# Optimization experiments

Hardware: AMD Instinct MI355X
Metric: run time of the kernel (lower is better)

Reference implementation:

```python
import jax, jax.numpy as jnp
import numpy as np

B, S, D = 4, 2048, 1024
H, ADIM = 16, 64
HID = H * ADIM  # 1024


def setup_inputs() -> dict:
    key = jax.random.key(0)
    k1, k2, k3, k4 = jax.random.split(key, 4)
    iQ = jax.random.normal(k1, (B, S, D), dtype=jnp.float32)
    mask = jax.random.randint(k2, (B, S, S), 0, 2).astype(bool)
    Wa = jax.random.normal(k3, (3 * HID, D), dtype=jnp.float32) * (1.0 / np.sqrt(D))
    Wo = jax.random.normal(k4, (HID, HID), dtype=jnp.float32) * (1.0 / np.sqrt(HID))
    return {"iQ": iQ, "mask": mask, "Wa": Wa, "Wo": Wo}


def reference(iQ, mask, Wa, Wo):
    b, s, _ = iQ.shape
    # fused QKV projection: [B,S,3*HID]
    qkv = jnp.einsum("bsd,ed->bse", iQ, Wa)
    q, k, v = jnp.split(qkv, 3, axis=-1)
    # [B,S,HID] -> [B,H,S,ADIM]
    to_heads = lambda t: t.reshape(b, s, H, ADIM).transpose(0, 2, 1, 3)
    q, k, v = to_heads(q), to_heads(k), to_heads(v)
    scores = jnp.einsum("bhqd,bhkd->bhqk", q, k) / np.sqrt(ADIM).astype(np.float32)
    scores = jnp.where(mask[:, None, :, :], jnp.float32(-1e32), scores)
    attn = jax.nn.softmax(scores, axis=-1)
    o = jnp.einsum("bhqk,bhkd->bhqd", attn, v)
    o = o.transpose(0, 2, 1, 3).reshape(b, s, HID)
    return jnp.einsum("bse,oe->bso", o, Wo)
```

## Files before the change

kernel.cpp:

```cpp
#include <hip/hip_runtime.h>
#include <hip/hip_bf16.h>

typedef __bf16 bf16;
typedef __bf16 bfrag __attribute__((ext_vector_type(8)));
typedef __bf16 bf16x2 __attribute__((ext_vector_type(2)));
typedef float f32x4 __attribute__((ext_vector_type(4)));
typedef float f32x16 __attribute__((ext_vector_type(16)));
typedef unsigned u32x2 __attribute__((ext_vector_type(2)));

constexpr int Bc = 4, Sc = 2048, Hc = 16, ADc = 64, HIDc = 1024;
constexpr size_t QKV_ELEMS = (size_t)Bc * Hc * Sc * ADc;

__device__ __forceinline__ void gload_lds16(const void* g, void* lds) {
  __builtin_amdgcn_global_load_lds(
      (const __attribute__((address_space(1))) unsigned int*)g,
      (__attribute__((address_space(3))) unsigned int*)lds, 16, 0, 0);
}

__device__ __forceinline__ bfrag ldb(const bf16* p) {
  return *(const bfrag*)p;
}

__device__ __forceinline__ unsigned pack2(float lo, float hi) {
  union { bf16x2 h; unsigned u; } c;
  c.h = bf16x2{(bf16)lo, (bf16)hi};
  return c.u;
}

__device__ __forceinline__ void plswap(unsigned& a, unsigned& b) {
  u32x2 r = __builtin_amdgcn_permlane32_swap(a, b, false, false);
  a = r.x;
  b = r.y;
}

__device__ __forceinline__ f32x16 zero16() {
  f32x16 z;
#pragma unroll
  for (int i = 0; i < 16; ++i) z[i] = 0.f;
  return z;
}

__global__ __launch_bounds__(256) void prep(const float* __restrict__ s0,
                                            const float* __restrict__ s1,
                                            const float* __restrict__ s2,
                                            bf16* __restrict__ d0,
                                            bf16* __restrict__ d1,
                                            bf16* __restrict__ d2,
                                            const int* __restrict__ mask,
                                            unsigned* __restrict__ bits) {
  const int blk = blockIdx.x;
  if (blk < 6144) {
    const float* s;
    bf16* d;
    size_t base;
    if (blk < 4096)      { s = s0; d = d0; base = (size_t)blk * 2048; }
    else if (blk < 5632) { s = s1; d = d1; base = (size_t)(blk - 4096) * 2048; }
    else                 { s = s2; d = d2; base = (size_t)(blk - 5632) * 2048; }
    const size_t i = base + (size_t)threadIdx.x * 8;
    const float4 a = *(const float4*)(s + i);
    const float4 b = *(const float4*)(s + i + 4);
    bfrag o = {(bf16)a.x, (bf16)a.y, (bf16)a.z, (bf16)a.w,
               (bf16)b.x, (bf16)b.y, (bf16)b.z, (bf16)b.w};
    *(bfrag*)(d + i) = o;
  } else {
    const int w = (blk - 6144) * 256 + threadIdx.x;
    const int4* p = (const int4*)(mask + (size_t)w * 32);
    unsigned out = 0;
#pragma unroll
    for (int i = 0; i < 8; ++i) {
      int4 m = p[i];
      out |= (unsigned)(m.x != 0) << (i * 4);
      out |= (unsigned)(m.y != 0) << (i * 4 + 1);
      out |= (unsigned)(m.z != 0) << (i * 4 + 2);
      out |= (unsigned)(m.w != 0) << (i * 4 + 3);
    }
    bits[w] = out;
  }
}

template <int MODE>
__global__ __launch_bounds__(256) void gemm_bt(
    const bf16* __restrict__ A,
    const bf16* __restrict__ Bm,
    bf16* __restrict__ C0,
    bf16* __restrict__ C1,
    bf16* __restrict__ C2,
    float* __restrict__ Cf,
    int Kdim, int Ndim)
{
  __shared__ __align__(16) bf16 As[128 * 32];
  __shared__ __align__(16) bf16 Bs[128 * 32];

  const int tid  = threadIdx.x;
  const int wave = tid >> 6;
  const int lane = tid & 63;
  const int n16  = lane & 15;
  const int quad = lane >> 4;
  const int wm   = wave & 1;
  const int wn   = wave >> 1;
  const int bid  = blockIdx.y * gridDim.x + blockIdx.x;
  const int nwg  = gridDim.x * gridDim.y;
  const int swz  = (bid & 7) * (nwg >> 3) + (bid >> 3);
  const int m0   = (swz / gridDim.x) * 128;
  const int n0   = (swz % gridDim.x) * 128;

  const f32x4 fzero = {0.f, 0.f, 0.f, 0.f};
  f32x4 acc[4][4];
#pragma unroll
  for (int i = 0; i < 4; ++i)
#pragma unroll
    for (int j = 0; j < 4; ++j) acc[i][j] = fzero;

  const int lcol = (lane & 3) * 8;

  for (int k0 = 0; k0 < Kdim; k0 += 32) {
#pragma unroll
    for (int c = 0; c < 2; ++c) {
      const int chunk = wave * 2 + c;
      const int row   = chunk * 16 + (lane >> 2);
      const bf16* agp;
      if (MODE == 0) {
        agp = A + (size_t)(m0 + row) * Kdim + k0 + lcol;
      } else {
        const int gs = m0 + row;
        const int h  = k0 >> 6;
        agp = A + (((size_t)(gs >> 11) * Hc + h) * Sc + (gs & 2047)) * ADc
                + (k0 & 63) + lcol;
      }
      gload_lds16(agp, (char*)As + chunk * 1024);
      gload_lds16(Bm + (size_t)(n0 + row) * Kdim + k0 + lcol,
                  (char*)Bs + chunk * 1024);
    }
    __syncthreads();

    bfrag af[4], bf[4];
#pragma unroll
    for (int i = 0; i < 4; ++i)
      af[i] = ldb(As + (wm * 64 + i * 16 + n16) * 32 + quad * 8);
#pragma unroll
    for (int j = 0; j < 4; ++j)
      bf[j] = ldb(Bs + (wn * 64 + j * 16 + n16) * 32 + quad * 8);
#pragma unroll
    for (int i = 0; i < 4; ++i)
#pragma unroll
      for (int j = 0; j < 4; ++j)
        acc[i][j] = __builtin_amdgcn_mfma_f32_16x16x32_bf16(af[i], bf[j], acc[i][j], 0, 0, 0);
    __syncthreads();
  }

#pragma unroll
  for (int i = 0; i < 4; ++i) {
    const int grow = m0 + wm * 64 + i * 16 + quad * 4;
#pragma unroll
    for (int j = 0; j < 4; ++j) {
      const int col_local = wn * 64 + j * 16 + n16;
#pragma unroll
      for (int r = 0; r < 4; ++r) {
        const int row = grow + r;
        const float v = acc[i][j][r];
        if (MODE == 1) {
          Cf[(size_t)row * Ndim + n0 + col_local] = v;
        } else {
          const int seg = n0 >> 10;
          const int hid = (n0 & 1023) + col_local;
          const int h = hid >> 6, a = hid & 63;
          const int bi = row >> 11, s = row & 2047;
          if (seg == 0)
            C0[(((size_t)bi * Hc + h) * Sc + s) * ADc + a] = (bf16)(v * 0.18033688011112042f);
          else if (seg == 1)
            C1[(((size_t)bi * Hc + h) * Sc + s) * ADc + a] = (bf16)v;
          else
            C2[(((size_t)bi * Hc + h) * ADc + a) * Sc + s] = (bf16)v;
        }
      }
    }
  }
}

__global__ __launch_bounds__(512, 4) void attn(
    const bf16* __restrict__ Qw,
    const bf16* __restrict__ Kw,
    const bf16* __restrict__ Vtw,
    const unsigned* __restrict__ mbits,
    bf16* __restrict__ Ow)
{
  __shared__ __align__(16) bf16 Ks[2][2][64 * 64];
  __shared__ __align__(16) bf16 Vs[2][2][64 * 64];

  const int tid  = threadIdx.x;
  const int wave = tid >> 6, lane = tid & 63;
  const int l31  = lane & 31, hi = lane >> 5;
  const int sw   = lane & 7;
  const int bh   = blockIdx.x & 63, qb = blockIdx.x >> 6;
  const int b    = bh >> 4;
  const int q0w  = qb * 256 + wave * 32;

  const int drow = wave * 8 + (lane >> 3);
  const int dchk = ((lane & 7) ^ (lane >> 3)) * 8;
  const bf16* gK = Kw  + ((size_t)bh * Sc + drow) * ADc + dchk;
  const bf16* gV = Vtw + ((size_t)bh * ADc + drow) * Sc + dchk;
  const int ldsb = wave * 1024;

  const bf16* qrow = Qw + ((size_t)bh * Sc + q0w + l31) * ADc + hi * 8;
  bfrag qf[4];
#pragma unroll
  for (int ks = 0; ks < 4; ++ks) qf[ks] = ldb(qrow + ks * 16);

  bfrag onef;
#pragma unroll
  for (int i = 0; i < 8; ++i) onef[i] = (bf16)1.0f;

  f32x16 of0  = zero16();
  f32x16 of1  = zero16();
  f32x16 dacc = zero16();

  const unsigned* mq = mbits + ((size_t)b * Sc + q0w + l31) * (Sc / 32);

  auto tile_compute = [&](const bf16* Kbuf, const bf16* Vbuf, unsigned mx,
                          unsigned my) {
#pragma unroll
    for (int nt = 0; nt < 2; ++nt) {
      f32x16 sf = zero16();
#pragma unroll
      for (int ks = 0; ks < 4; ++ks) {
        const bfrag kf = ldb(Kbuf + (nt * 32 + l31) * 64 + (((2 * ks + hi) ^ sw) * 8));
        sf = __builtin_amdgcn_mfma_f32_32x32x16_bf16(kf, qf[ks], sf, 0, 0, 0);
      }

      const unsigned w = (nt ? my : mx) >> (hi * 4);
      unsigned D[8];
#pragma unroll
      for (int m = 0; m < 8; ++m) {
        const int r0 = 2 * m, r1 = r0 + 1;
        float p0 = __builtin_amdgcn_exp2f(sf[r0]);
        float p1 = __builtin_amdgcn_exp2f(sf[r1]);
        if ((w >> ((r0 & 3) + 8 * (r0 >> 2))) & 1u) p0 = 0.f;
        if ((w >> ((r1 & 3) + 8 * (r1 >> 2))) & 1u) p1 = 0.f;
        D[m] = pack2(p0, p1);
      }

#pragma unroll
      for (int a = 0; a < 2; ++a) {
        unsigned w0 = D[4 * a + 0], w2 = D[4 * a + 2];
        plswap(w0, w2);
        unsigned w1 = D[4 * a + 1], w3 = D[4 * a + 3];
        plswap(w1, w3);
        union { unsigned u[4]; bfrag f; } pu;
        pu.u[0] = w0; pu.u[1] = w1; pu.u[2] = w2; pu.u[3] = w3;
        const int vg = ((4 * nt + 2 * a + hi) ^ sw) * 8;
        const bfrag vf0 = ldb(Vbuf + l31 * 64 + vg);
        of0 = __builtin_amdgcn_mfma_f32_32x32x16_bf16(pu.f, vf0, of0, 0, 0, 0);
        const bfrag vf1 = ldb(Vbuf + (32 + l31) * 64 + vg);
        of1 = __builtin_amdgcn_mfma_f32_32x32x16_bf16(pu.f, vf1, of1, 0, 0, 0);
        dacc = __builtin_amdgcn_mfma_f32_32x32x16_bf16(pu.f, onef, dacc, 0, 0, 0);
      }
    }
  };

  auto stage = [&](int buf, int kt) {
    const bf16* k0 = gK + (size_t)kt * 128 * ADc;
    const bf16* v0 = gV + (size_t)kt * 128;
    gload_lds16(k0,            (char*)Ks[buf][0] + ldsb);
    gload_lds16(k0 + 64 * ADc, (char*)Ks[buf][1] + ldsb);
    gload_lds16(v0,            (char*)Vs[buf][0] + ldsb);
    gload_lds16(v0 + 64,       (char*)Vs[buf][1] + ldsb);
  };

  stage(0, 0);
  __syncthreads();

  for (int kt = 0; kt < Sc / 128; ++kt) {
    const int cur = kt & 1;
    if (kt + 1 < Sc / 128) stage(cur ^ 1, kt + 1);

    const uint4 mwv = *(const uint4*)(mq + kt * 4);
    tile_compute(Ks[cur][0], Vs[cur][0], mwv.x, mwv.y);
    tile_compute(Ks[cur][1], Vs[cur][1], mwv.z, mwv.w);

    __syncthreads();
  }

#pragma unroll
  for (int r = 0; r < 16; ++r) {
    const int query = (r & 3) + 8 * (r >> 2) + 4 * hi;
    const float invr = 1.f / dacc[r];
    bf16* orow = Ow + ((size_t)bh * Sc + q0w + query) * ADc + l31;
    orow[0]  = (bf16)(of0[r] * invr);
    orow[32] = (bf16)(of1[r] * invr);
  }
}

extern "C" void kernel_launch(void* const* d_in, const int* in_sizes, int n_in,
                              void* d_out, int out_size, void* d_ws, size_t ws_size,
                              hipStream_t stream) {
  const float* iQ = (const float*)d_in[0];
  const int* mask = (const int*)d_in[1];
  const float* Wa = (const float*)d_in[2];
  const float* Wo = (const float*)d_in[3];
  float* out      = (float*)d_out;

  bf16* iQb       = (bf16*)d_out;
  bf16* Wab       = iQb + QKV_ELEMS;
  unsigned* mbits = (unsigned*)(Wab + 3145728);
  bf16* Qw  = (bf16*)d_ws;
  bf16* Kw  = Qw + QKV_ELEMS;
  bf16* Vtw = Kw + QKV_ELEMS;
  bf16* Wob = Vtw + QKV_ELEMS;

  prep<<<dim3(8192), 256, 0, stream>>>(iQ, Wa, Wo, iQb, Wab, Wob, mask, mbits);
  gemm_bt<0><<<dim3(24, 64), 256, 0, stream>>>(iQb, Wab, Qw, Kw, Vtw, nullptr, 1024, 3072);
  attn<<<dim3(Bc * Hc * 8), 512, 0, stream>>>(Qw, Kw, Vtw, mbits, Qw);
  gemm_bt<1><<<dim3(8, 64), 256, 0, stream>>>(Qw, Wob, nullptr, nullptr, nullptr, out, 1024, 1024);
}
```

Before: 366.2 us.

## Double GEMM K-tile to 64 with XOR-swizzled LDS and vectorized V^T stores

The projection GEMM now stages 64-wide K tiles per iteration instead of 32, halving the number of barrier pairs per K loop. LDS rows are XOR-swizzled in 16-byte groups so fragment reads avoid bank conflicts. The transposed V output is written as 4-element bf16 vectors along the sequence dimension instead of scalar strided stores. LDS use per block doubles, which may reduce occupancy.

```diff
diff --git a/kernel.cpp b/kernel.cpp
--- a/kernel.cpp
+++ b/kernel.cpp
@@ -4,6 +4,7 @@
 typedef __bf16 bf16;
 typedef __bf16 bfrag __attribute__((ext_vector_type(8)));
 typedef __bf16 bf16x2 __attribute__((ext_vector_type(2)));
+typedef __bf16 bf16x4 __attribute__((ext_vector_type(4)));
 typedef float f32x4 __attribute__((ext_vector_type(4)));
 typedef float f32x16 __attribute__((ext_vector_type(16)));
 typedef unsigned u32x2 __attribute__((ext_vector_type(2)));
@@ -88,8 +89,8 @@
     float* __restrict__ Cf,
     int Kdim, int Ndim)
 {
-  __shared__ __align__(16) bf16 As[128 * 32];
-  __shared__ __align__(16) bf16 Bs[128 * 32];
+  __shared__ __align__(16) bf16 As[128 * 64];
+  __shared__ __align__(16) bf16 Bs[128 * 64];
 
   const int tid  = threadIdx.x;
   const int wave = tid >> 6;
@@ -111,40 +112,44 @@
 #pragma unroll
     for (int j = 0; j < 4; ++j) acc[i][j] = fzero;
 
-  const int lcol = (lane & 3) * 8;
-
-  for (int k0 = 0; k0 < Kdim; k0 += 32) {
-#pragma unroll
-    for (int c = 0; c < 2; ++c) {
-      const int chunk = wave * 2 + c;
-      const int row   = chunk * 16 + (lane >> 2);
+  const int srow8 = tid >> 3;
+  const int dg    = (((tid & 7) ^ ((tid >> 3) & 7))) * 8;
+  const int fsw   = n16 & 7;
+
+  for (int k0 = 0; k0 < Kdim; k0 += 64) {
+#pragma unroll
+    for (int c = 0; c < 4; ++c) {
+      const int arow = c * 32 + srow8;
       const bf16* agp;
       if (MODE == 0) {
-        agp = A + (size_t)(m0 + row) * Kdim + k0 + lcol;
+        agp = A + (size_t)(m0 + arow) * Kdim + k0 + dg;
       } else {
-        const int gs = m0 + row;
+        const int gs = m0 + arow;
         const int h  = k0 >> 6;
-        agp = A + (((size_t)(gs >> 11) * Hc + h) * Sc + (gs & 2047)) * ADc
-                + (k0 & 63) + lcol;
-      }
-      gload_lds16(agp, (char*)As + chunk * 1024);
-      gload_lds16(Bm + (size_t)(n0 + row) * Kdim + k0 + lcol,
-                  (char*)Bs + chunk * 1024);
+        agp = A + (((size_t)(gs >> 11) * Hc + h) * Sc + (gs & 2047)) * ADc + dg;
+      }
+      gload_lds16(agp, (char*)As + wave * 1024 + c * 4096);
+      gload_lds16(Bm + (size_t)(n0 + arow) * Kdim + k0 + dg,
+                  (char*)Bs + wave * 1024 + c * 4096);
     }
     __syncthreads();
 
-    bfrag af[4], bf[4];
-#pragma unroll
-    for (int i = 0; i < 4; ++i)
-      af[i] = ldb(As + (wm * 64 + i * 16 + n16) * 32 + quad * 8);
-#pragma unroll
-    for (int j = 0; j < 4; ++j)
-      bf[j] = ldb(Bs + (wn * 64 + j * 16 + n16) * 32 + quad * 8);
-#pragma unroll
-    for (int i = 0; i < 4; ++i)
+#pragma unroll
+    for (int ks = 0; ks < 2; ++ks) {
+      const int go = ((ks * 4 + quad) ^ fsw) * 8;
+      bfrag af[4], bf[4];
+#pragma unroll
+      for (int i = 0; i < 4; ++i)
+        af[i] = ldb(As + (wm * 64 + i * 16 + n16) * 64 + go);
 #pragma unroll
       for (int j = 0; j < 4; ++j)
-        acc[i][j] = __builtin_amdgcn_mfma_f32_16x16x32_bf16(af[i], bf[j], acc[i][j], 0, 0, 0);
+        bf[j] = ldb(Bs + (wn * 64 + j * 16 + n16) * 64 + go);
+#pragma unroll
+      for (int i = 0; i < 4; ++i)
+#pragma unroll
+        for (int j = 0; j < 4; ++j)
+          acc[i][j] = __builtin_amdgcn_mfma_f32_16x16x32_bf16(af[i], bf[j], acc[i][j], 0, 0, 0);
+    }
     __syncthreads();
   }
 
@@ -154,23 +159,31 @@
 #pragma unroll
     for (int j = 0; j < 4; ++j) {
       const int col_local = wn * 64 + j * 16 + n16;
-#pragma unroll
-      for (int r = 0; r < 4; ++r) {
-        const int row = grow + r;
-        const float v = acc[i][j][r];
-        if (MODE == 1) {
-          Cf[(size_t)row * Ndim + n0 + col_local] = v;
-        } else {
-          const int seg = n0 >> 10;
-          const int hid = (n0 & 1023) + col_local;
-          const int h = hid >> 6, a = hid & 63;
-          const int bi = row >> 11, s = row & 2047;
-          if (seg == 0)
-            C0[(((size_t)bi * Hc + h) * Sc + s) * ADc + a] = (bf16)(v * 0.18033688011112042f);
-          else if (seg == 1)
-            C1[(((size_t)bi * Hc + h) * Sc + s) * ADc + a] = (bf16)v;
-          else
-            C2[(((size_t)bi * Hc + h) * ADc + a) * Sc + s] = (bf16)v;
+      const int seg = n0 >> 10;
+      if (MODE == 0 && seg == 2) {
+        const int hid = (n0 & 1023) + col_local;
+        const int h = hid >> 6, a = hid & 63;
+        const int bi = grow >> 11, s0 = grow & 2047;
+        bf16x4 v4;
+#pragma unroll
+        for (int r = 0; r < 4; ++r) v4[r] = (bf16)acc[i][j][r];
+        *(bf16x4*)(C2 + (((size_t)bi * Hc + h) * ADc + a) * Sc + s0) = v4;
+      } else {
+#pragma unroll
+        for (int r = 0; r < 4; ++r) {
+          const int row = grow + r;
+          const float v = acc[i][j][r];
+          if (MODE == 1) {
+            Cf[(size_t)row * Ndim + n0 + col_local] = v;
+          } else {
+            const int hid = (n0 & 1023) + col_local;
+            const int h = hid >> 6, a = hid & 63;
+            const int bi = row >> 11, s = row & 2047;
+            if (seg == 0)
+              C0[(((size_t)bi * Hc + h) * Sc + s) * ADc + a] = (bf16)(v * 0.18033688011112042f);
+            else
+              C1[(((size_t)bi * Hc + h) * Sc + s) * ADc + a] = (bf16)v;
+          }
         }
       }
     }
```

Measured after the change: 337.6 us. 1.08x faster.

## Double-buffer GEMM LDS tiles and vectorize transposed V stores

Applied to the files above, without the earlier changes.

The GEMM kernel now keeps two LDS buffers per operand and issues the global-to-LDS loads for the next K slice before running the MFMAs on the current one, so load latency can overlap compute and one barrier per iteration is dropped. The transposed V output path now packs four consecutive sequence elements into a single 8-byte store instead of four scattered 2-byte stores. LDS use per block doubles, which can lower occupancy. The prefetch into the other buffer is issued without waiting on the loads for the current one, which depends on the async LDS load ordering being safe.

```diff
diff --git a/kernel.cpp b/kernel.cpp
--- a/kernel.cpp
+++ b/kernel.cpp
@@ -4,6 +4,7 @@
 typedef __bf16 bf16;
 typedef __bf16 bfrag __attribute__((ext_vector_type(8)));
 typedef __bf16 bf16x2 __attribute__((ext_vector_type(2)));
+typedef __bf16 bf16x4 __attribute__((ext_vector_type(4)));
 typedef float f32x4 __attribute__((ext_vector_type(4)));
 typedef float f32x16 __attribute__((ext_vector_type(16)));
 typedef unsigned u32x2 __attribute__((ext_vector_type(2)));
@@ -88,8 +89,8 @@
     float* __restrict__ Cf,
     int Kdim, int Ndim)
 {
-  __shared__ __align__(16) bf16 As[128 * 32];
-  __shared__ __align__(16) bf16 Bs[128 * 32];
+  __shared__ __align__(16) bf16 As[2][128 * 32];
+  __shared__ __align__(16) bf16 Bs[2][128 * 32];
 
   const int tid  = threadIdx.x;
   const int wave = tid >> 6;
@@ -112,12 +113,13 @@
     for (int j = 0; j < 4; ++j) acc[i][j] = fzero;
 
   const int lcol = (lane & 3) * 8;
-
-  for (int k0 = 0; k0 < Kdim; k0 += 32) {
+  const int srow = lane >> 2;
+
+  auto stage = [&](int buf, int k0) {
 #pragma unroll
     for (int c = 0; c < 2; ++c) {
       const int chunk = wave * 2 + c;
-      const int row   = chunk * 16 + (lane >> 2);
+      const int row   = chunk * 16 + srow;
       const bf16* agp;
       if (MODE == 0) {
         agp = A + (size_t)(m0 + row) * Kdim + k0 + lcol;
@@ -127,24 +129,32 @@
         agp = A + (((size_t)(gs >> 11) * Hc + h) * Sc + (gs & 2047)) * ADc
                 + (k0 & 63) + lcol;
       }
-      gload_lds16(agp, (char*)As + chunk * 1024);
+      gload_lds16(agp, (char*)As[buf] + chunk * 1024);
       gload_lds16(Bm + (size_t)(n0 + row) * Kdim + k0 + lcol,
-                  (char*)Bs + chunk * 1024);
+                  (char*)Bs[buf] + chunk * 1024);
     }
-    __syncthreads();
+  };
+
+  stage(0, 0);
+  __syncthreads();
+
+  for (int k0 = 0; k0 < Kdim; k0 += 32) {
+    const int cur = (k0 >> 5) & 1;
+    if (k0 + 32 < Kdim) stage(cur ^ 1, k0 + 32);
 
     bfrag af[4], bf[4];
 #pragma unroll
     for (int i = 0; i < 4; ++i)
-      af[i] = ldb(As + (wm * 64 + i * 16 + n16) * 32 + quad * 8);
+      af[i] = ldb(As[cur] + (wm * 64 + i * 16 + n16) * 32 + quad * 8);
 #pragma unroll
     for (int j = 0; j < 4; ++j)
-      bf[j] = ldb(Bs + (wn * 64 + j * 16 + n16) * 32 + quad * 8);
+      bf[j] = ldb(Bs[cur] + (wn * 64 + j * 16 + n16) * 32 + quad * 8);
 #pragma unroll
     for (int i = 0; i < 4; ++i)
 #pragma unroll
       for (int j = 0; j < 4; ++j)
         acc[i][j] = __builtin_amdgcn_mfma_f32_16x16x32_bf16(af[i], bf[j], acc[i][j], 0, 0, 0);
+
     __syncthreads();
   }
 
@@ -154,23 +164,31 @@
 #pragma unroll
     for (int j = 0; j < 4; ++j) {
       const int col_local = wn * 64 + j * 16 + n16;
-#pragma unroll
-      for (int r = 0; r < 4; ++r) {
-        const int row = grow + r;
-        const float v = acc[i][j][r];
-        if (MODE == 1) {
-          Cf[(size_t)row * Ndim + n0 + col_local] = v;
-        } else {
-          const int seg = n0 >> 10;
-          const int hid = (n0 & 1023) + col_local;
-          const int h = hid >> 6, a = hid & 63;
-          const int bi = row >> 11, s = row & 2047;
-          if (seg == 0)
-            C0[(((size_t)bi * Hc + h) * Sc + s) * ADc + a] = (bf16)(v * 0.18033688011112042f);
-          else if (seg == 1)
-            C1[(((size_t)bi * Hc + h) * Sc + s) * ADc + a] = (bf16)v;
-          else
-            C2[(((size_t)bi * Hc + h) * ADc + a) * Sc + s] = (bf16)v;
+      const int seg = n0 >> 10;
+      if (MODE == 0 && seg == 2) {
+        const int hid = (n0 & 1023) + col_local;
+        const int h = hid >> 6, a = hid & 63;
+        const int bi = grow >> 11, s0 = grow & 2047;
+        bf16x4 v4;
+#pragma unroll
+        for (int r = 0; r < 4; ++r) v4[r] = (bf16)acc[i][j][r];
+        *(bf16x4*)(C2 + (((size_t)bi * Hc + h) * ADc + a) * Sc + s0) = v4;
+      } else {
+#pragma unroll
+        for (int r = 0; r < 4; ++r) {
+          const int row = grow + r;
+          const float v = acc[i][j][r];
+          if (MODE == 1) {
+            Cf[(size_t)row * Ndim + n0 + col_local] = v;
+          } else {
+            const int hid = (n0 & 1023) + col_local;
+            const int h = hid >> 6, a = hid & 63;
+            const int bi = row >> 11, s = row & 2047;
+            if (seg == 0)
+              C0[(((size_t)bi * Hc + h) * Sc + s) * ADc + a] = (bf16)(v * 0.18033688011112042f);
+            else
+              C1[(((size_t)bi * Hc + h) * Sc + s) * ADc + a] = (bf16)v;
+          }
         }
       }
     }
```

Result: faster. 327.7 us (-10.5%).
